# Optimization experiments

Hardware: AMD Instinct MI355X
Metric: run time of the kernel (lower is better)

## Reference

```python
import jax, jax.numpy as jnp
import numpy as np

# dims
N, BARS, F = 1024, 64, 32          # frames, bars per frame, bar features
H, HEADS, ENC_L, FFN = 256, 8, 4, 1024
HD = H // HEADS
D, DS, DC, ML = 512, 16, 4, 8      # mamba d_model, d_state, d_conv, n_layers
DI = 2 * D                          # expand=2 -> d_inner
DR = D // 16                        # dt_rank
HID = 128                           # VIX head hidden


def _ln(x, g, b, eps=1e-5):
    m = x.mean(-1, keepdims=True)
    v = ((x - m) ** 2).mean(-1, keepdims=True)
    return (x - m) * jax.lax.rsqrt(v + eps) * g + b


def setup_inputs() -> dict:
    key = jax.random.key(0)
    ks = iter(jax.random.split(key, 64))
    r = lambda *s: jax.random.normal(next(ks), s, jnp.float32) * 0.02
    inp = {}
    inp['frames'] = jax.random.normal(next(ks), (N, BARS, F), jnp.float32)
    inp['frame_mask'] = jnp.ones((N, BARS), jnp.float32)
    # bar encoder (transformer)
    inp['in_w'] = r(F, H); inp['in_b'] = jnp.zeros((H,), jnp.float32)
    inp['pos_emb'] = r(BARS, H)
    inp['enc_qkv_w'] = r(ENC_L, H, 3 * H); inp['enc_qkv_b'] = jnp.zeros((ENC_L, 3 * H), jnp.float32)
    inp['enc_attn_out_w'] = r(ENC_L, H, H); inp['enc_attn_out_b'] = jnp.zeros((ENC_L, H), jnp.float32)
    inp['enc_ln1_g'] = jnp.ones((ENC_L, H), jnp.float32); inp['enc_ln1_b'] = jnp.zeros((ENC_L, H), jnp.float32)
    inp['enc_ffn_w1'] = r(ENC_L, H, FFN); inp['enc_ffn_b1'] = jnp.zeros((ENC_L, FFN), jnp.float32)
    inp['enc_ffn_w2'] = r(ENC_L, FFN, H); inp['enc_ffn_b2'] = jnp.zeros((ENC_L, H), jnp.float32)
    inp['enc_ln2_g'] = jnp.ones((ENC_L, H), jnp.float32); inp['enc_ln2_b'] = jnp.zeros((ENC_L, H), jnp.float32)
    # projection hidden_dim -> d_model
    inp['proj_w'] = r(H, D); inp['proj_b'] = jnp.zeros((D,), jnp.float32)
    # mamba stack (stacked over ML layers)
    inp['m_in_w'] = r(ML, D, 2 * DI)
    inp['m_conv_w'] = r(ML, DI, DC); inp['m_conv_b'] = jnp.zeros((ML, DI), jnp.float32)
    inp['m_xproj_w'] = r(ML, DI, DR + 2 * DS)
    inp['m_dt_w'] = r(ML, DR, DI)
    inp['m_dt_b'] = jnp.full((ML, DI), -4.6, jnp.float32)  # softplus(-4.6)~0.01
    inp['m_Alog'] = jnp.broadcast_to(jnp.log(jnp.arange(1, DS + 1, dtype=jnp.float32)), (ML, DI, DS)) + 0.0
    inp['m_D'] = jnp.ones((ML, DI), jnp.float32)
    inp['m_out_w'] = r(ML, DI, D)
    inp['m_ln_g'] = jnp.ones((ML, D), jnp.float32); inp['m_ln_b'] = jnp.zeros((ML, D), jnp.float32)
    # attention pooling
    inp['pool_w'] = r(D, 1); inp['pool_b'] = jnp.zeros((1,), jnp.float32)
    # VIX head
    inp['h1_w'] = r(D, HID); inp['h1_b'] = jnp.zeros((HID,), jnp.float32)
    inp['hln1_g'] = jnp.ones((HID,), jnp.float32); inp['hln1_b'] = jnp.zeros((HID,), jnp.float32)
    inp['h2_w'] = r(HID, HID); inp['h2_b'] = jnp.zeros((HID,), jnp.float32)
    inp['hln2_g'] = jnp.ones((HID,), jnp.float32); inp['hln2_b'] = jnp.zeros((HID,), jnp.float32)
    inp['h3_w'] = r(HID, 1); inp['h3_b'] = jnp.zeros((1,), jnp.float32)
    return inp


def _forward(frames, frame_mask, in_w, in_b, pos_emb, enc_qkv_w, enc_qkv_b,
             enc_attn_out_w, enc_attn_out_b, enc_ln1_g, enc_ln1_b,
             enc_ffn_w1, enc_ffn_b1, enc_ffn_w2, enc_ffn_b2, enc_ln2_g, enc_ln2_b,
             proj_w, proj_b, m_in_w, m_conv_w, m_conv_b, m_xproj_w, m_dt_w, m_dt_b,
             m_Alog, m_D, m_out_w, m_ln_g, m_ln_b, pool_w, pool_b,
             h1_w, h1_b, hln1_g, hln1_b, h2_w, h2_b, hln2_g, hln2_b, h3_w, h3_b):
    # ---- bar encoder: per-frame transformer over bars ----
    x = frames @ in_w + in_b + pos_emb                        # [N,BARS,H]
    bias = (1.0 - frame_mask)[:, None, None, :] * -1e9        # key padding mask
    scale = 1.0 / np.sqrt(HD)
    for l in range(ENC_L):
        qkv = x @ enc_qkv_w[l] + enc_qkv_b[l]
        q, k, v = jnp.split(qkv, 3, axis=-1)
        q = q.reshape(N, BARS, HEADS, HD)
        k = k.reshape(N, BARS, HEADS, HD)
        v = v.reshape(N, BARS, HEADS, HD)
        att = jnp.einsum('nqhd,nkhd->nhqk', q, k) * scale + bias
        att = jax.nn.softmax(att, axis=-1)
        o = jnp.einsum('nhqk,nkhd->nqhd', att, v).reshape(N, BARS, H)
        x = _ln(x + o @ enc_attn_out_w[l] + enc_attn_out_b[l], enc_ln1_g[l], enc_ln1_b[l])
        f = jax.nn.gelu(x @ enc_ffn_w1[l] + enc_ffn_b1[l], approximate=False) @ enc_ffn_w2[l] + enc_ffn_b2[l]
        x = _ln(x + f, enc_ln2_g[l], enc_ln2_b[l])
    m = frame_mask[..., None]
    frame_emb = (x * m).sum(1) / jnp.clip(m.sum(1), 1.0)      # [N,H] masked mean pool

    # ---- project to d_model; sequence of frames is the Mamba sequence (B=1) ----
    x = frame_emb @ proj_w + proj_b                           # [T,D], T=N
    for l in range(ML):
        res = x
        xi, z = jnp.split(x @ m_in_w[l], 2, axis=-1)          # [T,DI] each
        # causal depthwise conv1d, kernel DC
        xp = jnp.pad(xi, ((DC - 1, 0), (0, 0)))
        xw = jnp.stack([xp[k:k + N] for k in range(DC)], axis=-1)  # [T,DI,DC]
        xc = jax.nn.silu((xw * m_conv_w[l]).sum(-1) + m_conv_b[l])
        xdbl = xc @ m_xproj_w[l]                               # [T,DR+2*DS]
        dtr, Bm, Cm = xdbl[:, :DR], xdbl[:, DR:DR + DS], xdbl[:, DR + DS:]
        dt = jax.nn.softplus(dtr @ m_dt_w[l] + m_dt_b[l])      # [T,DI]
        A = -jnp.exp(m_Alog[l])                                # [DI,DS]
        dA = jnp.exp(dt[:, :, None] * A)                       # [T,DI,DS]
        dBx = dt[:, :, None] * Bm[:, None, :] * xc[:, :, None] # [T,DI,DS]

        def step(h, inp):
            dA_t, dBx_t, C_t = inp
            h = h * dA_t + dBx_t
            return h, h @ C_t                                  # y_t [DI]
        _, ys = jax.lax.scan(step, jnp.zeros((DI, DS), x.dtype), (dA, dBx, Cm))
        y = (ys + m_D[l] * xc) * jax.nn.silu(z)
        x = _ln(y @ m_out_w[l], m_ln_g[l], m_ln_b[l]) + res    # layer -> norm -> +residual

    # ---- attention pooling (no mask at this stage, matches forward()) ----
    w = jax.nn.softmax(x @ pool_w + pool_b, axis=0)            # [T,1]
    hp = (w * x).sum(0)                                        # [D]
    # ---- VIX head ----
    t = jax.nn.gelu(_ln(hp @ h1_w + h1_b, hln1_g, hln1_b), approximate=False)
    t = jax.nn.gelu(_ln(t @ h2_w + h2_b, hln2_g, hln2_b), approximate=False)
    vix = t @ h3_w + h3_b                                      # [1] (batch of 1)
    return vix, x[None]                                        # vix_pred, mamba_hidden [1,T,D]


def reference(frames, frame_mask, in_w, in_b, pos_emb, enc_qkv_w, enc_qkv_b,
              enc_attn_out_w, enc_attn_out_b, enc_ln1_g, enc_ln1_b,
              enc_ffn_w1, enc_ffn_b1, enc_ffn_w2, enc_ffn_b2, enc_ln2_g, enc_ln2_b,
              proj_w, proj_b, m_in_w, m_conv_w, m_conv_b, m_xproj_w, m_dt_w, m_dt_b,
              m_Alog, m_D, m_out_w, m_ln_g, m_ln_b, pool_w, pool_b,
              h1_w, h1_b, hln1_g, hln1_b, h2_w, h2_b, hln2_g, hln2_b, h3_w, h3_b):
    return _forward(frames, frame_mask, in_w, in_b, pos_emb, enc_qkv_w, enc_qkv_b,
                    enc_attn_out_w, enc_attn_out_b, enc_ln1_g, enc_ln1_b,
                    enc_ffn_w1, enc_ffn_b1, enc_ffn_w2, enc_ffn_b2, enc_ln2_g, enc_ln2_b,
                    proj_w, proj_b, m_in_w, m_conv_w, m_conv_b, m_xproj_w, m_dt_w, m_dt_b,
                    m_Alog, m_D, m_out_w, m_ln_g, m_ln_b, pool_w, pool_b,
                    h1_w, h1_b, hln1_g, hln1_b, h2_w, h2_b, hln2_g, hln2_b, h3_w, h3_b)
```

## Files before the change

### kernel.cpp

```cpp
#include <hip/hip_runtime.h>
#include <math.h>

#define ACT_NONE 0
#define ACT_GELU 1
#define ACT_SOFTPLUS 2

template<int ACT>
__device__ __forceinline__ float act_apply(float x){
  if (ACT == ACT_GELU)     return 0.5f * x * (1.0f + erff(x * 0.70710678118654752f));
  if (ACT == ACT_SOFTPLUS) return fmaxf(x, 0.0f) + log1pf(expf(-fabsf(x)));
  return x;
}

__device__ __forceinline__ unsigned short f2bf(float x){
  unsigned u = __float_as_uint(x);
  u = u + 0x7FFFu + ((u >> 16) & 1u);
  return (unsigned short)(u >> 16);
}
__device__ __forceinline__ float bf2f(unsigned short b){
  return __uint_as_float(((unsigned)b) << 16);
}
__device__ __forceinline__ void bfsplit(float x, unsigned short &hi, unsigned short &lo){
  hi = f2bf(x);
  lo = f2bf(x - bf2f(hi));
}

typedef __attribute__((ext_vector_type(8))) short v8s;
typedef __attribute__((ext_vector_type(4))) float v4f;

template<int ACT, int OUT>
__global__ __launch_bounds__(256) void gemm_bf16x2_kernel(
    const unsigned short* __restrict__ Ahi, const unsigned short* __restrict__ Alo,
    const unsigned short* __restrict__ Bhi, const unsigned short* __restrict__ Blo,
    const float* __restrict__ bias, float* __restrict__ C,
    unsigned short* __restrict__ Chi, unsigned short* __restrict__ Clo,
    int K, int lda, int ldb, int ldc)
{
  __shared__ unsigned short As[2][128][40];
  __shared__ unsigned short Bs[2][128][40];
  const int tid = threadIdx.x;
  const int m0 = blockIdx.y * 128;
  const int n0 = blockIdx.x * 128;
  const int w = tid >> 6, lane = tid & 63;
  const int wm = (w & 1) * 64, wn = (w >> 1) * 64;
  const int fm = lane & 15, fq = lane >> 4;
  const int r = tid >> 1, h = tid & 1;

  const unsigned short* pAh = Ahi + (size_t)(m0 + r) * lda + h * 16;
  const unsigned short* pAl = Alo + (size_t)(m0 + r) * lda + h * 16;
  const unsigned short* pBh = Bhi + (size_t)(n0 + r) * ldb + h * 16;
  const unsigned short* pBl = Blo + (size_t)(n0 + r) * ldb + h * 16;

  v4f acc[4][4];
#pragma unroll
  for (int i = 0; i < 4; i++)
#pragma unroll
    for (int j = 0; j < 4; j++) acc[i][j] = (v4f){0.f, 0.f, 0.f, 0.f};

  uint4 ah0 = *(const uint4*)(pAh),     ah1 = *(const uint4*)(pAh + 8);
  uint4 al0 = *(const uint4*)(pAl),     al1 = *(const uint4*)(pAl + 8);
  uint4 bh0 = *(const uint4*)(pBh),     bh1 = *(const uint4*)(pBh + 8);
  uint4 bl0 = *(const uint4*)(pBl),     bl1 = *(const uint4*)(pBl + 8);

  for (int k0 = 0; k0 < K; k0 += 32) {
    __syncthreads();
    *(uint4*)&As[0][r][h * 16]     = ah0;
    *(uint4*)&As[0][r][h * 16 + 8] = ah1;
    *(uint4*)&As[1][r][h * 16]     = al0;
    *(uint4*)&As[1][r][h * 16 + 8] = al1;
    *(uint4*)&Bs[0][r][h * 16]     = bh0;
    *(uint4*)&Bs[0][r][h * 16 + 8] = bh1;
    *(uint4*)&Bs[1][r][h * 16]     = bl0;
    *(uint4*)&Bs[1][r][h * 16 + 8] = bl1;
    __syncthreads();

    if (k0 + 32 < K) {
      int kn = k0 + 32;
      ah0 = *(const uint4*)(pAh + kn); ah1 = *(const uint4*)(pAh + kn + 8);
      al0 = *(const uint4*)(pAl + kn); al1 = *(const uint4*)(pAl + kn + 8);
      bh0 = *(const uint4*)(pBh + kn); bh1 = *(const uint4*)(pBh + kn + 8);
      bl0 = *(const uint4*)(pBl + kn); bl1 = *(const uint4*)(pBl + kn + 8);
    }

    v8s ah[4], al[4];
#pragma unroll
    for (int i = 0; i < 4; i++) {
      ah[i] = *(const v8s*)&As[0][wm + i * 16 + fm][fq * 8];
      al[i] = *(const v8s*)&As[1][wm + i * 16 + fm][fq * 8];
    }
#pragma unroll
    for (int j = 0; j < 4; j++) {
      v8s bh = *(const v8s*)&Bs[0][wn + j * 16 + fm][fq * 8];
      v8s bl = *(const v8s*)&Bs[1][wn + j * 16 + fm][fq * 8];
#pragma unroll
      for (int i = 0; i < 4; i++) {
        acc[i][j] = __builtin_amdgcn_mfma_f32_16x16x32_bf16(ah[i], bh, acc[i][j], 0, 0, 0);
        acc[i][j] = __builtin_amdgcn_mfma_f32_16x16x32_bf16(ah[i], bl, acc[i][j], 0, 0, 0);
        acc[i][j] = __builtin_amdgcn_mfma_f32_16x16x32_bf16(al[i], bh, acc[i][j], 0, 0, 0);
      }
    }
  }

#pragma unroll
  for (int i = 0; i < 4; i++)
#pragma unroll
    for (int j = 0; j < 4; j++) {
      int col = n0 + wn + j * 16 + fm;
      float bv = bias ? bias[col] : 0.0f;
#pragma unroll
      for (int reg = 0; reg < 4; reg++) {
        int row = m0 + wm + i * 16 + fq * 4 + reg;
        float v = acc[i][j][reg] + bv;
        v = act_apply<ACT>(v);
        size_t idx = (size_t)row * ldc + col;
        if (OUT == 0) C[idx] = v;
        else { unsigned short hi, lo; bfsplit(v, hi, lo); Chi[idx] = hi; Clo[idx] = lo; }
      }
    }
}

__global__ __launch_bounds__(256) void gemm_ln_kernel(
    const unsigned short* __restrict__ Ahi, const unsigned short* __restrict__ Alo,
    const unsigned short* __restrict__ Bhi, const unsigned short* __restrict__ Blo,
    const float* __restrict__ bias,
    const float* __restrict__ g, const float* __restrict__ beta,
    unsigned short* __restrict__ Xhi, unsigned short* __restrict__ Xlo,
    int K, int lda, int ldb)
{
  __shared__ unsigned short As[2][32][40];
  __shared__ unsigned short Bs[2][256][40];
  __shared__ float rs[32][5];
  __shared__ float ms[32][2];
  const int tid = threadIdx.x;
  const int m0 = blockIdx.x * 32;
  const int w = tid >> 6, lane = tid & 63;
  const int fm = lane & 15, fq = lane >> 4;
  const int a_sel = tid >> 7;
  const int a_row = (tid >> 2) & 31;
  const int a_c   = tid & 3;
  const int b_row = tid >> 2;
  const int b_c   = tid & 3;

  v4f acc[2][4];
#pragma unroll
  for (int i = 0; i < 2; i++)
#pragma unroll
    for (int j = 0; j < 4; j++) acc[i][j] = (v4f){0.f, 0.f, 0.f, 0.f};

  for (int k0 = 0; k0 < K; k0 += 32) {
    __syncthreads();
    {
      const unsigned short* asrc = (a_sel ? Alo : Ahi) + (size_t)(m0 + a_row) * lda + k0 + a_c * 8;
      *(uint4*)&As[a_sel][a_row][a_c * 8] = *(const uint4*)asrc;
    }
#pragma unroll
    for (int p = 0; p < 4; p++) {
      int row = p * 64 + b_row;
      *(uint4*)&Bs[0][row][b_c * 8] = *(const uint4*)(Bhi + (size_t)row * ldb + k0 + b_c * 8);
      *(uint4*)&Bs[1][row][b_c * 8] = *(const uint4*)(Blo + (size_t)row * ldb + k0 + b_c * 8);
    }
    __syncthreads();

    v8s ah[2], al[2];
#pragma unroll
    for (int i = 0; i < 2; i++) {
      ah[i] = *(const v8s*)&As[0][i * 16 + fm][fq * 8];
      al[i] = *(const v8s*)&As[1][i * 16 + fm][fq * 8];
    }
#pragma unroll
    for (int j = 0; j < 4; j++) {
      v8s bhf = *(const v8s*)&Bs[0][w * 64 + j * 16 + fm][fq * 8];
      v8s blf = *(const v8s*)&Bs[1][w * 64 + j * 16 + fm][fq * 8];
#pragma unroll
      for (int i = 0; i < 2; i++) {
        acc[i][j] = __builtin_amdgcn_mfma_f32_16x16x32_bf16(ah[i], bhf, acc[i][j], 0, 0, 0);
        acc[i][j] = __builtin_amdgcn_mfma_f32_16x16x32_bf16(ah[i], blf, acc[i][j], 0, 0, 0);
        acc[i][j] = __builtin_amdgcn_mfma_f32_16x16x32_bf16(al[i], bhf, acc[i][j], 0, 0, 0);
      }
    }
  }

#pragma unroll
  for (int i = 0; i < 2; i++)
#pragma unroll
    for (int j = 0; j < 4; j++) {
      int cl = w * 64 + j * 16 + fm;
      float bv = bias[cl];
#pragma unroll
      for (int reg = 0; reg < 4; reg++) {
        int rl = i * 16 + fq * 4 + reg;
        size_t idx = (size_t)(m0 + rl) * 256 + cl;
        acc[i][j][reg] += bv + bf2f(Xhi[idx]) + bf2f(Xlo[idx]);
      }
    }
#pragma unroll
  for (int i = 0; i < 2; i++)
#pragma unroll
    for (int reg = 0; reg < 4; reg++) {
      float s = acc[i][0][reg] + acc[i][1][reg] + acc[i][2][reg] + acc[i][3][reg];
      s += __shfl_xor(s, 1); s += __shfl_xor(s, 2);
      s += __shfl_xor(s, 4); s += __shfl_xor(s, 8);
      if (fm == 0) rs[i * 16 + fq * 4 + reg][w] = s;
    }
  __syncthreads();
  if (tid < 32) ms[tid][0] = (rs[tid][0] + rs[tid][1] + rs[tid][2] + rs[tid][3]) * (1.0f / 256.0f);
  __syncthreads();
#pragma unroll
  for (int i = 0; i < 2; i++)
#pragma unroll
    for (int reg = 0; reg < 4; reg++) {
      int rl = i * 16 + fq * 4 + reg;
      float mean = ms[rl][0];
      float s = 0.0f;
#pragma unroll
      for (int j = 0; j < 4; j++) { float d = acc[i][j][reg] - mean; s += d * d; }
      s += __shfl_xor(s, 1); s += __shfl_xor(s, 2);
      s += __shfl_xor(s, 4); s += __shfl_xor(s, 8);
      if (fm == 0) rs[rl][w] = s;
    }
  __syncthreads();
  if (tid < 32) {
    float var = (rs[tid][0] + rs[tid][1] + rs[tid][2] + rs[tid][3]) * (1.0f / 256.0f);
    ms[tid][1] = rsqrtf(var + 1e-5f);
  }
  __syncthreads();
#pragma unroll
  for (int i = 0; i < 2; i++)
#pragma unroll
    for (int j = 0; j < 4; j++) {
      int cl = w * 64 + j * 16 + fm;
      float gv = g[cl], bv = beta[cl];
#pragma unroll
      for (int reg = 0; reg < 4; reg++) {
        int rl = i * 16 + fq * 4 + reg;
        float t = (acc[i][j][reg] - ms[rl][0]) * ms[rl][1] * gv + bv;
        size_t idx = (size_t)(m0 + rl) * 256 + cl;
        unsigned short hi, lo; bfsplit(t, hi, lo);
        Xhi[idx] = hi; Xlo[idx] = lo;
      }
    }
}

__global__ __launch_bounds__(256) void wsplit_kernel(
    const float* __restrict__ W, unsigned short* __restrict__ Whi,
    unsigned short* __restrict__ Wlo, int K, int N, size_t wstride, size_t ostride)
{
  __shared__ float tile[32][33];
  const float* Wl = W + blockIdx.z * wstride;
  unsigned short* Whl = Whi + blockIdx.z * ostride;
  unsigned short* Wll = Wlo + blockIdx.z * ostride;
  int k0 = blockIdx.y * 32, n0 = blockIdx.x * 32;
  int t = threadIdx.x;
  int tn = t & 31, tk8 = t >> 5;
#pragma unroll
  for (int i = 0; i < 4; i++) {
    int k = tk8 + i * 8;
    tile[k][tn] = Wl[(size_t)(k0 + k) * N + n0 + tn];
  }
  __syncthreads();
  int tk = t & 31, tn8 = t >> 5;
#pragma unroll
  for (int i = 0; i < 4; i++) {
    int n = tn8 + i * 8;
    float v = tile[tk][n];
    unsigned short hi, lo; bfsplit(v, hi, lo);
    size_t idx = (size_t)(n0 + n) * K + k0 + tk;
    Whl[idx] = hi; Wll[idx] = lo;
  }
}

template<int ACT, int POS, int SPLIT>
__global__ __launch_bounds__(256) void gemm128_kernel(
    const float* __restrict__ A, const float* __restrict__ W,
    const float* __restrict__ bias, const float* __restrict__ pos,
    float* __restrict__ C, unsigned short* __restrict__ Chi, unsigned short* __restrict__ Clo,
    int K, int lda, int ldw, int ldc)
{
  __shared__ float As[16][128];
  __shared__ float Ws[16][128];
  const int tid = threadIdx.x;
  const int m0 = blockIdx.y * 128;
  const int n0 = blockIdx.x * 128;
  const int tx = tid & 15, ty = tid >> 4;
  const int ar = tid >> 2, ak = (tid & 3) * 4;
  const int wk = tid >> 5, wn = (tid & 31) * 4;

  float acc[8][8];
#pragma unroll
  for (int i = 0; i < 8; i++)
#pragma unroll
    for (int j = 0; j < 8; j++) acc[i][j] = 0.0f;

  for (int k0 = 0; k0 < K; k0 += 16) {
    float4 a0 = *(const float4*)(A + (size_t)(m0 + ar)      * lda + k0 + ak);
    float4 a1 = *(const float4*)(A + (size_t)(m0 + ar + 64) * lda + k0 + ak);
    float4 w0 = *(const float4*)(W + (size_t)(k0 + wk)     * ldw + n0 + wn);
    float4 w1 = *(const float4*)(W + (size_t)(k0 + wk + 8) * ldw + n0 + wn);
    __syncthreads();
    As[ak + 0][ar] = a0.x; As[ak + 1][ar] = a0.y; As[ak + 2][ar] = a0.z; As[ak + 3][ar] = a0.w;
    As[ak + 0][ar + 64] = a1.x; As[ak + 1][ar + 64] = a1.y; As[ak + 2][ar + 64] = a1.z; As[ak + 3][ar + 64] = a1.w;
    *(float4*)&Ws[wk][wn] = w0;
    *(float4*)&Ws[wk + 8][wn] = w1;
    __syncthreads();
#pragma unroll
    for (int k = 0; k < 16; k++) {
      float4 xa = *(float4*)&As[k][ty * 8];
      float4 xb = *(float4*)&As[k][ty * 8 + 4];
      float4 y0 = *(float4*)&Ws[k][tx * 8];
      float4 y1 = *(float4*)&Ws[k][tx * 8 + 4];
      float a8[8] = {xa.x, xa.y, xa.z, xa.w, xb.x, xb.y, xb.z, xb.w};
      float b8[8] = {y0.x, y0.y, y0.z, y0.w, y1.x, y1.y, y1.z, y1.w};
#pragma unroll
      for (int i = 0; i < 8; i++)
#pragma unroll
        for (int j = 0; j < 8; j++) acc[i][j] = fmaf(a8[i], b8[j], acc[i][j]);
    }
  }
#pragma unroll
  for (int i = 0; i < 8; i++) {
    int row = m0 + ty * 8 + i;
    float* cp = C + (size_t)row * ldc + n0 + tx * 8;
    float v[8];
#pragma unroll
    for (int j = 0; j < 8; j++) {
      float t = acc[i][j];
      int col = n0 + tx * 8 + j;
      if (bias) t += bias[col];
      if (POS)  t += pos[(row & 63) * 256 + col];
      t = act_apply<ACT>(t);
      v[j] = t;
      if (SPLIT) {
        unsigned short hi, lo; bfsplit(t, hi, lo);
        size_t idx = (size_t)row * ldc + col;
        Chi[idx] = hi; Clo[idx] = lo;
      }
    }
    *(float4*)cp       = make_float4(v[0], v[1], v[2], v[3]);
    *(float4*)(cp + 4) = make_float4(v[4], v[5], v[6], v[7]);
  }
}

template<int ACT>
__global__ __launch_bounds__(256) void gemm64_kernel(
    const float* __restrict__ A, const float* __restrict__ W,
    const float* __restrict__ bias, float* __restrict__ C,
    int K, int lda, int ldw, int ldc)
{
  __shared__ float As[16][64];
  __shared__ float Ws[16][64];
  const int tid = threadIdx.x;
  const int m0 = blockIdx.y * 64;
  const int n0 = blockIdx.x * 64;
  const int tx = tid & 15, ty = tid >> 4;
  const int ar = tid >> 2, ak = (tid & 3) * 4;
  const int wk = tid >> 4, wn = (tid & 15) * 4;

  float acc[4][4];
#pragma unroll
  for (int i = 0; i < 4; i++)
#pragma unroll
    for (int j = 0; j < 4; j++) acc[i][j] = 0.0f;

  float4 a0 = *(const float4*)(A + (size_t)(m0 + ar) * lda + ak);
  float4 w0 = *(const float4*)(W + (size_t)wk * ldw + n0 + wn);

  for (int k0 = 0; k0 < K; k0 += 16) {
    __syncthreads();
    As[ak + 0][ar] = a0.x; As[ak + 1][ar] = a0.y; As[ak + 2][ar] = a0.z; As[ak + 3][ar] = a0.w;
    *(float4*)&Ws[wk][wn] = w0;
    __syncthreads();
    if (k0 + 16 < K) {
      a0 = *(const float4*)(A + (size_t)(m0 + ar) * lda + k0 + 16 + ak);
      w0 = *(const float4*)(W + (size_t)(k0 + 16 + wk) * ldw + n0 + wn);
    }
#pragma unroll
    for (int k = 0; k < 16; k++) {
      float4 xa = *(float4*)&As[k][ty * 4];
      float4 yb = *(float4*)&Ws[k][tx * 4];
      float a4[4] = {xa.x, xa.y, xa.z, xa.w};
      float b4[4] = {yb.x, yb.y, yb.z, yb.w};
#pragma unroll
      for (int i = 0; i < 4; i++)
#pragma unroll
        for (int j = 0; j < 4; j++) acc[i][j] = fmaf(a4[i], b4[j], acc[i][j]);
    }
  }
#pragma unroll
  for (int i = 0; i < 4; i++) {
    float* cp = C + (size_t)(m0 + ty * 4 + i) * ldc + n0 + tx * 4;
    float v[4];
#pragma unroll
    for (int j = 0; j < 4; j++) {
      float t = acc[i][j];
      if (bias) t += bias[n0 + tx * 4 + j];
      v[j] = act_apply<ACT>(t);
    }
    *(float4*)cp = make_float4(v[0], v[1], v[2], v[3]);
  }
}

__global__ __launch_bounds__(64) void attn_fused_kernel(
    const float* __restrict__ QKVc, const float* __restrict__ mask,
    unsigned short* __restrict__ AThi, unsigned short* __restrict__ ATlo, int n0)
{
  int bid = blockIdx.x;
  int nl = bid >> 3;
  int h = bid & 7;
  int n = n0 + nl;
  int tid = threadIdx.x;
  int tx = tid & 7, ty = tid >> 3;
  __shared__ float Qt[32][68];
  __shared__ float Kt[32][68];
  __shared__ float Vs[64][36];
  __shared__ float Pt[64][68];
  __shared__ float bs[64];
  const float* base = QKVc + (size_t)nl * (64 * 768);
#pragma unroll
  for (int i = 0; i < 32; i++) {
    int idx = tid + i * 64;
    int bar = idx >> 5, c = idx & 31;
    Qt[c][bar] = base[bar * 768 + h * 32 + c];
    Kt[c][bar] = base[bar * 768 + 256 + h * 32 + c];
    Vs[bar][c] = base[bar * 768 + 512 + h * 32 + c];
  }
  bs[tid] = (1.0f - mask[n * 64 + tid]) * -1e9f;
  __syncthreads();
  float acc[8][8] = {};
  for (int c = 0; c < 32; c++) {
    float4 ax = *(float4*)&Qt[c][ty * 8];
    float4 ay = *(float4*)&Qt[c][ty * 8 + 4];
    float4 bx = *(float4*)&Kt[c][tx * 8];
    float4 by = *(float4*)&Kt[c][tx * 8 + 4];
    float a8[8] = {ax.x, ax.y, ax.z, ax.w, ay.x, ay.y, ay.z, ay.w};
    float b8[8] = {bx.x, bx.y, bx.z, bx.w, by.x, by.y, by.z, by.w};
#pragma unroll
    for (int i = 0; i < 8; i++)
#pragma unroll
      for (int j = 0; j < 8; j++) acc[i][j] = fmaf(a8[i], b8[j], acc[i][j]);
  }
  const float scale = 0.17677669529663687f;
#pragma unroll
  for (int i = 0; i < 8; i++) {
    float s[8];
    float mx = -3.0e38f;
#pragma unroll
    for (int j = 0; j < 8; j++) { s[j] = acc[i][j] * scale + bs[tx * 8 + j]; mx = fmaxf(mx, s[j]); }
#pragma unroll
    for (int off = 1; off < 8; off <<= 1) mx = fmaxf(mx, __shfl_xor(mx, off));
    float sum = 0.0f;
#pragma unroll
    for (int j = 0; j < 8; j++) { s[j] = expf(s[j] - mx); sum += s[j]; }
#pragma unroll
    for (int off = 1; off < 8; off <<= 1) sum += __shfl_xor(sum, off);
    float inv = 1.0f / sum;
#pragma unroll
    for (int j = 0; j < 8; j++) Pt[tx * 8 + j][ty * 8 + i] = s[j] * inv;
  }
  __syncthreads();
  float o[8][4] = {};
  for (int j = 0; j < 64; j++) {
    float4 px = *(float4*)&Pt[j][ty * 8];
    float4 py = *(float4*)&Pt[j][ty * 8 + 4];
    float4 v  = *(float4*)&Vs[j][tx * 4];
    float p8[8] = {px.x, px.y, px.z, px.w, py.x, py.y, py.z, py.w};
#pragma unroll
    for (int i = 0; i < 8; i++) {
      o[i][0] = fmaf(p8[i], v.x, o[i][0]);
      o[i][1] = fmaf(p8[i], v.y, o[i][1]);
      o[i][2] = fmaf(p8[i], v.z, o[i][2]);
      o[i][3] = fmaf(p8[i], v.w, o[i][3]);
    }
  }
#pragma unroll
  for (int i = 0; i < 8; i++) {
    size_t base_o = (size_t)(nl * 64 + ty * 8 + i) * 256 + h * 32 + tx * 4;
#pragma unroll
    for (int c = 0; c < 4; c++) {
      unsigned short hi, lo; bfsplit(o[i][c], hi, lo);
      AThi[base_o + c] = hi; ATlo[base_o + c] = lo;
    }
  }
}

__global__ __launch_bounds__(256) void ln_res_kernel(
    const float* __restrict__ a, const float* __restrict__ b,
    const float* __restrict__ g, const float* __restrict__ beta,
    float* __restrict__ o, int Wd)
{
  int wave = threadIdx.x >> 6;
  int lane = threadIdx.x & 63;
  int row = blockIdx.x * 4 + wave;
  int P = Wd >> 6;
  const float* ar = a + (size_t)row * Wd;
  const float* br = b + (size_t)row * Wd;
  float v[8];
  float s = 0.0f;
  for (int i = 0; i < P; i++) { float x = ar[lane + i * 64]; v[i] = x; s += x; }
#pragma unroll
  for (int off = 32; off; off >>= 1) s += __shfl_xor(s, off);
  float mean = s / Wd;
  float vs = 0.0f;
  for (int i = 0; i < P; i++) { float d = v[i] - mean; vs += d * d; }
#pragma unroll
  for (int off = 32; off; off >>= 1) vs += __shfl_xor(vs, off);
  float rstd = rsqrtf(vs / Wd + 1e-5f);
  for (int i = 0; i < P; i++) {
    int col = lane + i * 64;
    o[(size_t)row * Wd + col] = (v[i] - mean) * rstd * g[col] + beta[col] + br[col];
  }
}

__global__ __launch_bounds__(256) void mean_kernel(
    const unsigned short* __restrict__ Xhi, const unsigned short* __restrict__ Xlo,
    const float* __restrict__ mask, float* __restrict__ FE, int n0)
{
  int n = blockIdx.x;
  int c = threadIdx.x;
  float s = 0.0f, ms = 0.0f;
  for (int bar = 0; bar < 64; bar++) {
    float mk = mask[(n0 + n) * 64 + bar];
    size_t idx = (size_t)(n * 64 + bar) * 256 + c;
    s = fmaf(bf2f(Xhi[idx]) + bf2f(Xlo[idx]), mk, s);
    ms += mk;
  }
  FE[(n0 + n) * 256 + c] = s / fmaxf(ms, 1.0f);
}

__global__ __launch_bounds__(256) void conv_kernel(
    const float* __restrict__ XZ, const float* __restrict__ w,
    const float* __restrict__ b, float* __restrict__ XC)
{
  int idx = blockIdx.x * 256 + threadIdx.x;
  int t = idx >> 10, c = idx & 1023;
  float acc = b[c];
  const float* wc = w + c * 4;
#pragma unroll
  for (int k = 0; k < 4; k++) {
    int tt = t + k - 3;
    if (tt >= 0) acc = fmaf(XZ[(size_t)tt * 2048 + c], wc[k], acc);
  }
  XC[idx] = acc / (1.0f + expf(-acc));
}

#define NCH 32
#define CLEN 32

__global__ __launch_bounds__(256) void scan1_kernel(
    const float* __restrict__ DT, const float* __restrict__ XC,
    const float* __restrict__ XDBL, const float* __restrict__ Alog,
    float* __restrict__ HEND, float* __restrict__ PPR)
{
  int j = blockIdx.x >> 2;
  int c = (blockIdx.x & 3) * 256 + threadIdx.x;
  int t0 = j * CLEN;
  __shared__ float Bs[CLEN][16];
  for (int i = threadIdx.x; i < CLEN * 16; i += 256) {
    int r = i >> 4, s = i & 15;
    Bs[r][s] = XDBL[(t0 + r) * 64 + 32 + s];
  }
  float A[16], h[16], Pp[16];
#pragma unroll
  for (int s = 0; s < 16; s++) {
    A[s] = -expf(Alog[c * 16 + s]);
    h[s] = 0.0f; Pp[s] = 1.0f;
  }
  __syncthreads();
  for (int tt = 0; tt < CLEN; tt++) {
    int t = t0 + tt;
    float dtv = DT[(size_t)t * 1024 + c];
    float u = dtv * XC[(size_t)t * 1024 + c];
#pragma unroll
    for (int s = 0; s < 16; s++) {
      float e = expf(dtv * A[s]);
      h[s] = fmaf(h[s], e, u * Bs[tt][s]);
      Pp[s] *= e;
    }
  }
#pragma unroll
  for (int s = 0; s < 16; s++) {
    HEND[(size_t)(j * 1024 + c) * 16 + s] = h[s];
    PPR [(size_t)(j * 1024 + c) * 16 + s] = Pp[s];
  }
}

__global__ __launch_bounds__(256) void scan2_kernel(
    const float* __restrict__ HEND, const float* __restrict__ PPR, float* __restrict__ CIN)
{
  int id = blockIdx.x * 256 + threadIdx.x;
  float carry = 0.0f;
  for (int j = 0; j < NCH; j++) {
    CIN[j * 16384 + id] = carry;
    carry = fmaf(PPR[j * 16384 + id], carry, HEND[j * 16384 + id]);
  }
}

__global__ __launch_bounds__(256) void scan3_kernel(
    const float* __restrict__ DT, const float* __restrict__ XC,
    const float* __restrict__ XDBL, const float* __restrict__ Alog,
    const float* __restrict__ CIN, const float* __restrict__ mD,
    const float* __restrict__ XZ, float* __restrict__ Y)
{
  int j = blockIdx.x >> 2;
  int c = (blockIdx.x & 3) * 256 + threadIdx.x;
  int t0 = j * CLEN;
  __shared__ float Bs[CLEN][16], Cs[CLEN][16];
  for (int i = threadIdx.x; i < CLEN * 16; i += 256) {
    int r = i >> 4, s = i & 15;
    Bs[r][s] = XDBL[(t0 + r) * 64 + 32 + s];
    Cs[r][s] = XDBL[(t0 + r) * 64 + 48 + s];
  }
  float A[16], h[16];
#pragma unroll
  for (int s = 0; s < 16; s++) {
    A[s] = -expf(Alog[c * 16 + s]);
    h[s] = CIN[(size_t)(j * 1024 + c) * 16 + s];
  }
  float dval = mD[c];
  __syncthreads();
  for (int tt = 0; tt < CLEN; tt++) {
    int t = t0 + tt;
    float dtv = DT[(size_t)t * 1024 + c];
    float xcv = XC[(size_t)t * 1024 + c];
    float u = dtv * xcv;
    float y = 0.0f;
#pragma unroll
    for (int s = 0; s < 16; s++) {
      float e = expf(dtv * A[s]);
      h[s] = fmaf(h[s], e, u * Bs[tt][s]);
      y = fmaf(h[s], Cs[tt][s], y);
    }
    float z = XZ[(size_t)t * 2048 + 1024 + c];
    float sz = z / (1.0f + expf(-z));
    Y[(size_t)t * 1024 + c] = (y + dval * xcv) * sz;
  }
}

__global__ __launch_bounds__(1024) void pool1_kernel(
    const float* __restrict__ XM, const float* __restrict__ pw,
    const float* __restrict__ pb, float* __restrict__ PW)
{
  int t = threadIdx.x;
  float s = pb[0];
  for (int i = 0; i < 512; i++) s = fmaf(XM[(size_t)t * 512 + i], pw[i], s);
  __shared__ float red[1024];
  red[t] = s;
  __syncthreads();
  for (int off = 512; off > 0; off >>= 1) {
    if (t < off) red[t] = fmaxf(red[t], red[t + off]);
    __syncthreads();
  }
  float mx = red[0];
  __syncthreads();
  float e = expf(s - mx);
  red[t] = e;
  __syncthreads();
  for (int off = 512; off > 0; off >>= 1) {
    if (t < off) red[t] = red[t] + red[t + off];
    __syncthreads();
  }
  PW[t] = e / red[0];
}

__global__ __launch_bounds__(256) void pool2_kernel(
    const float* __restrict__ XM, const float* __restrict__ PW, float* __restrict__ HP)
{
  int hcol = blockIdx.x * 256 + threadIdx.x;
  float s = 0.0f;
  for (int tn = 0; tn < 1024; tn++) s = fmaf(PW[tn], XM[(size_t)tn * 512 + hcol], s);
  HP[hcol] = s;
}

__device__ __forceinline__ float blk_reduce_sum_128(float v, float* red){
  int t = threadIdx.x;
#pragma unroll
  for (int off = 32; off; off >>= 1) v += __shfl_xor(v, off);
  __syncthreads();
  if ((t & 63) == 0) red[t >> 6] = v;
  __syncthreads();
  return red[0] + red[1];
}

__global__ __launch_bounds__(128) void head_kernel(
    const float* __restrict__ HP, const float* __restrict__ h1w, const float* __restrict__ h1b,
    const float* __restrict__ g1, const float* __restrict__ be1,
    const float* __restrict__ h2w, const float* __restrict__ h2b,
    const float* __restrict__ g2, const float* __restrict__ be2,
    const float* __restrict__ h3w, const float* __restrict__ h3b,
    float* __restrict__ out)
{
  __shared__ float t1[128];
  __shared__ float red[2];
  int i = threadIdx.x;
  float s = h1b[i];
  for (int k = 0; k < 512; k++) s = fmaf(HP[k], h1w[k * 128 + i], s);
  float mean = blk_reduce_sum_128(s, red) * (1.0f / 128.0f);
  float d = s - mean;
  float var = blk_reduce_sum_128(d * d, red) * (1.0f / 128.0f);
  float x1 = d * rsqrtf(var + 1e-5f) * g1[i] + be1[i];
  x1 = 0.5f * x1 * (1.0f + erff(x1 * 0.70710678118654752f));
  t1[i] = x1;
  __syncthreads();
  s = h2b[i];
  for (int k = 0; k < 128; k++) s = fmaf(t1[k], h2w[k * 128 + i], s);
  mean = blk_reduce_sum_128(s, red) * (1.0f / 128.0f);
  d = s - mean;
  var = blk_reduce_sum_128(d * d, red) * (1.0f / 128.0f);
  float x2 = d * rsqrtf(var + 1e-5f) * g2[i] + be2[i];
  x2 = 0.5f * x2 * (1.0f + erff(x2 * 0.70710678118654752f));
  float tot = blk_reduce_sum_128(x2 * h3w[i], red);
  if (i == 0) out[0] = tot + h3b[0];
}

__global__ __launch_bounds__(256) void copyx_kernel(const float* __restrict__ XM, float* __restrict__ out){
  int i = blockIdx.x * 256 + threadIdx.x;
  out[1 + i] = XM[i];
}

extern "C" void kernel_launch(void* const* d_in, const int* in_sizes, int n_in,
                              void* d_out, int out_size, void* d_ws, size_t ws_size,
                              hipStream_t stream)
{
  const float* frames   = (const float*)d_in[0];
  const float* fmask    = (const float*)d_in[1];
  const float* in_w     = (const float*)d_in[2];
  const float* in_b     = (const float*)d_in[3];
  const float* pos_emb  = (const float*)d_in[4];
  const float* qkv_w    = (const float*)d_in[5];
  const float* qkv_b    = (const float*)d_in[6];
  const float* ao_w     = (const float*)d_in[7];
  const float* ao_b     = (const float*)d_in[8];
  const float* ln1_g    = (const float*)d_in[9];
  const float* ln1_b    = (const float*)d_in[10];
  const float* ffn_w1   = (const float*)d_in[11];
  const float* ffn_b1   = (const float*)d_in[12];
  const float* ffn_w2   = (const float*)d_in[13];
  const float* ffn_b2   = (const float*)d_in[14];
  const float* ln2_g    = (const float*)d_in[15];
  const float* ln2_b    = (const float*)d_in[16];
  const float* proj_w   = (const float*)d_in[17];
  const float* proj_b   = (const float*)d_in[18];
  const float* m_in_w   = (const float*)d_in[19];
  const float* m_conv_w = (const float*)d_in[20];
  const float* m_conv_b = (const float*)d_in[21];
  const float* m_xproj_w= (const float*)d_in[22];
  const float* m_dt_w   = (const float*)d_in[23];
  const float* m_dt_b   = (const float*)d_in[24];
  const float* m_Alog   = (const float*)d_in[25];
  const float* m_D      = (const float*)d_in[26];
  const float* m_out_w  = (const float*)d_in[27];
  const float* m_ln_g   = (const float*)d_in[28];
  const float* m_ln_b   = (const float*)d_in[29];
  const float* pool_w   = (const float*)d_in[30];
  const float* pool_b   = (const float*)d_in[31];
  const float* h1_w     = (const float*)d_in[32];
  const float* h1_b     = (const float*)d_in[33];
  const float* hg1      = (const float*)d_in[34];
  const float* hb1      = (const float*)d_in[35];
  const float* h2_w     = (const float*)d_in[36];
  const float* h2_b     = (const float*)d_in[37];
  const float* hg2      = (const float*)d_in[38];
  const float* hb2      = (const float*)d_in[39];
  const float* h3_w     = (const float*)d_in[40];
  const float* h3_b     = (const float*)d_in[41];
  float* out = (float*)d_out;

  float* ws = (float*)d_ws;
  float* B  = ws;
  float* QF = B;
  unsigned short* AThi = (unsigned short*)(B + 12582912);
  unsigned short* ATlo = AThi + 4194304;
  unsigned short* MIDhi = (unsigned short*)B;
  unsigned short* MIDlo = MIDhi + 16777216;

  unsigned short* Xhi = (unsigned short*)(ws + 16777216);
  unsigned short* Xlo = Xhi + 4194304;

  unsigned short* Wqkv_hi = (unsigned short*)(ws + 20971520);
  unsigned short* Wqkv_lo = Wqkv_hi + 786432;
  unsigned short* Wao_hi  = Wqkv_lo + 786432;
  unsigned short* Wao_lo  = Wao_hi + 262144;
  unsigned short* Wf1_hi  = Wao_lo + 262144;
  unsigned short* Wf1_lo  = Wf1_hi + 1048576;
  unsigned short* Wf2_hi  = Wf1_lo + 1048576;
  unsigned short* Wf2_lo  = Wf2_hi + 1048576;

  float* FE = ws + 24117248;
  float* XM = FE + 262144;
  float* PW = XM + 524288;
  float* HP = PW + 2048;

  float* XZ   = B;
  float* XC   = B + 2097152;
  float* DT   = B + 3145728;
  float* XDBL = B + 4194304;
  float* Y    = B + 4259840;
  float* TMP  = B + 5308416;
  float* HEND = B + 5832704;
  float* PPR  = B + 6356992;
  float* CIN  = B + 6881280;

  wsplit_kernel<<<dim3(24,8,4),256,0,stream>>>(qkv_w, Wqkv_hi, Wqkv_lo, 256, 768, 196608, 196608);
  wsplit_kernel<<<dim3(8,8,4),256,0,stream>>>(ao_w, Wao_hi, Wao_lo, 256, 256, 65536, 65536);
  wsplit_kernel<<<dim3(32,8,4),256,0,stream>>>(ffn_w1, Wf1_hi, Wf1_lo, 256, 1024, 262144, 262144);
  wsplit_kernel<<<dim3(8,32,4),256,0,stream>>>(ffn_w2, Wf2_hi, Wf2_lo, 1024, 256, 262144, 262144);

  for (int ch = 0; ch < 4; ch++) {
    int n0 = ch * 256;
    const float* fch = frames + (size_t)n0 * 64 * 32;
    gemm128_kernel<ACT_NONE,1,1><<<dim3(2,128),256,0,stream>>>(
        fch, in_w, in_b, pos_emb, QF, Xhi, Xlo, 32, 32, 256, 256);
    for (int l = 0; l < 4; l++) {
      gemm_bf16x2_kernel<ACT_NONE,0><<<dim3(6,128),256,0,stream>>>(
          Xhi, Xlo, Wqkv_hi + l*196608, Wqkv_lo + l*196608, qkv_b + l*768,
          QF, nullptr, nullptr, 256, 256, 256, 768);
      attn_fused_kernel<<<2048,64,0,stream>>>(QF, fmask, AThi, ATlo, n0);
      gemm_ln_kernel<<<512,256,0,stream>>>(
          AThi, ATlo, Wao_hi + l*65536, Wao_lo + l*65536, ao_b + l*256,
          ln1_g + l*256, ln1_b + l*256, Xhi, Xlo, 256, 256, 256);
      gemm_bf16x2_kernel<ACT_GELU,2><<<dim3(8,128),256,0,stream>>>(
          Xhi, Xlo, Wf1_hi + l*262144, Wf1_lo + l*262144, ffn_b1 + l*1024,
          nullptr, MIDhi, MIDlo, 256, 256, 256, 1024);
      gemm_ln_kernel<<<512,256,0,stream>>>(
          MIDhi, MIDlo, Wf2_hi + l*262144, Wf2_lo + l*262144, ffn_b2 + l*256,
          ln2_g + l*256, ln2_b + l*256, Xhi, Xlo, 1024, 1024, 1024);
    }
    mean_kernel<<<256,256,0,stream>>>(Xhi, Xlo, fmask, FE, n0);
  }

  gemm64_kernel<ACT_NONE><<<dim3(8,16),256,0,stream>>>(FE, proj_w, proj_b, XM, 256, 256, 512, 512);

  for (int l = 0; l < 8; l++) {
    gemm64_kernel<ACT_NONE><<<dim3(32,16),256,0,stream>>>(
        XM, m_in_w + (size_t)l*512*2048, nullptr, XZ, 512, 512, 2048, 2048);
    conv_kernel<<<4096,256,0,stream>>>(XZ, m_conv_w + l*1024*4, m_conv_b + l*1024, XC);
    gemm64_kernel<ACT_NONE><<<dim3(1,16),256,0,stream>>>(
        XC, m_xproj_w + (size_t)l*1024*64, nullptr, XDBL, 1024, 1024, 64, 64);
    gemm64_kernel<ACT_SOFTPLUS><<<dim3(16,16),256,0,stream>>>(
        XDBL, m_dt_w + (size_t)l*32*1024, m_dt_b + l*1024, DT, 32, 64, 1024, 1024);
    scan1_kernel<<<128,256,0,stream>>>(DT, XC, XDBL, m_Alog + l*16384, HEND, PPR);
    scan2_kernel<<<64,256,0,stream>>>(HEND, PPR, CIN);
    scan3_kernel<<<128,256,0,stream>>>(DT, XC, XDBL, m_Alog + l*16384, CIN, m_D + l*1024, XZ, Y);
    gemm64_kernel<ACT_NONE><<<dim3(8,16),256,0,stream>>>(
        Y, m_out_w + (size_t)l*1024*512, nullptr, TMP, 1024, 1024, 512, 512);
    ln_res_kernel<<<256,256,0,stream>>>(TMP, XM, m_ln_g + l*512, m_ln_b + l*512, XM, 512);
  }

  pool1_kernel<<<1,1024,0,stream>>>(XM, pool_w, pool_b, PW);
  pool2_kernel<<<2,256,0,stream>>>(XM, PW, HP);
  head_kernel<<<1,128,0,stream>>>(HP, h1_w, h1_b, hg1, hb1, h2_w, h2_b, hg2, hb2, h3_w, h3_b, out);
  copyx_kernel<<<2048,256,0,stream>>>(XM, out);
}
```

Measured before the change: 5.405 ms.

## Enlarge gemm_ln tile to 64 rows with 512 threads; alias attention smem

The GEMM+LayerNorm kernel now processes 64 rows per block with 8 waves instead of 32 rows with 4 waves. Each wave covers 32 output columns over 4 row fragments, so every loaded B (weight) tile is reused across twice as many rows, halving weight traffic per output row. The row-reduction scratch grows to match. Separately, the attention kernel now reuses the Q/K shared-memory region for the probability matrix, with an added barrier, to cut LDS footprint and raise occupancy. The trade-off is half as many blocks for the LN GEMMs (256) and more registers per thread.

Result: no change. 5.392 ms (-0.3%).

```diff
diff --git a/kernel.cpp b/kernel.cpp
--- a/kernel.cpp
+++ b/kernel.cpp
@@ -119,7 +119,7 @@
     }
 }
 
-__global__ __launch_bounds__(256) void gemm_ln_kernel(
+__global__ __launch_bounds__(512) void gemm_ln_kernel(
     const unsigned short* __restrict__ Ahi, const unsigned short* __restrict__ Alo,
     const unsigned short* __restrict__ Bhi, const unsigned short* __restrict__ Blo,
     const float* __restrict__ bias,
@@ -127,52 +127,50 @@
     unsigned short* __restrict__ Xhi, unsigned short* __restrict__ Xlo,
     int K, int lda, int ldb)
 {
-  __shared__ unsigned short As[2][32][40];
+  __shared__ unsigned short As[2][64][40];
   __shared__ unsigned short Bs[2][256][40];
-  __shared__ float rs[32][5];
-  __shared__ float ms[32][2];
+  __shared__ float rs[64][9];
+  __shared__ float ms[64][2];
   const int tid = threadIdx.x;
-  const int m0 = blockIdx.x * 32;
+  const int m0 = blockIdx.x * 64;
   const int w = tid >> 6, lane = tid & 63;
   const int fm = lane & 15, fq = lane >> 4;
-  const int a_sel = tid >> 7;
-  const int a_row = (tid >> 2) & 31;
+  const int a_pl  = tid >> 8;
+  const int a_row = (tid >> 2) & 63;
   const int a_c   = tid & 3;
   const int b_row = tid >> 2;
   const int b_c   = tid & 3;
 
-  v4f acc[2][4];
-#pragma unroll
-  for (int i = 0; i < 2; i++)
-#pragma unroll
-    for (int j = 0; j < 4; j++) acc[i][j] = (v4f){0.f, 0.f, 0.f, 0.f};
+  v4f acc[4][2];
+#pragma unroll
+  for (int i = 0; i < 4; i++)
+#pragma unroll
+    for (int j = 0; j < 2; j++) acc[i][j] = (v4f){0.f, 0.f, 0.f, 0.f};
 
   for (int k0 = 0; k0 < K; k0 += 32) {
     __syncthreads();
     {
-      const unsigned short* asrc = (a_sel ? Alo : Ahi) + (size_t)(m0 + a_row) * lda + k0 + a_c * 8;
-      *(uint4*)&As[a_sel][a_row][a_c * 8] = *(const uint4*)asrc;
-    }
-#pragma unroll
-    for (int p = 0; p < 4; p++) {
-      int row = p * 64 + b_row;
-      *(uint4*)&Bs[0][row][b_c * 8] = *(const uint4*)(Bhi + (size_t)row * ldb + k0 + b_c * 8);
-      *(uint4*)&Bs[1][row][b_c * 8] = *(const uint4*)(Blo + (size_t)row * ldb + k0 + b_c * 8);
-    }
-    __syncthreads();
-
-    v8s ah[2], al[2];
-#pragma unroll
-    for (int i = 0; i < 2; i++) {
+      const unsigned short* asrc = (a_pl ? Alo : Ahi) + (size_t)(m0 + a_row) * lda + k0 + a_c * 8;
+      *(uint4*)&As[a_pl][a_row][a_c * 8] = *(const uint4*)asrc;
+    }
+    *(uint4*)&Bs[0][b_row      ][b_c * 8] = *(const uint4*)(Bhi + (size_t)(b_row      ) * ldb + k0 + b_c * 8);
+    *(uint4*)&Bs[0][b_row + 128][b_c * 8] = *(const uint4*)(Bhi + (size_t)(b_row + 128) * ldb + k0 + b_c * 8);
+    *(uint4*)&Bs[1][b_row      ][b_c * 8] = *(const uint4*)(Blo + (size_t)(b_row      ) * ldb + k0 + b_c * 8);
+    *(uint4*)&Bs[1][b_row + 128][b_c * 8] = *(const uint4*)(Blo + (size_t)(b_row + 128) * ldb + k0 + b_c * 8);
+    __syncthreads();
+
+    v8s ah[4], al[4];
+#pragma unroll
+    for (int i = 0; i < 4; i++) {
       ah[i] = *(const v8s*)&As[0][i * 16 + fm][fq * 8];
       al[i] = *(const v8s*)&As[1][i * 16 + fm][fq * 8];
     }
 #pragma unroll
-    for (int j = 0; j < 4; j++) {
-      v8s bhf = *(const v8s*)&Bs[0][w * 64 + j * 16 + fm][fq * 8];
-      v8s blf = *(const v8s*)&Bs[1][w * 64 + j * 16 + fm][fq * 8];
-#pragma unroll
-      for (int i = 0; i < 2; i++) {
+    for (int j = 0; j < 2; j++) {
+      v8s bhf = *(const v8s*)&Bs[0][w * 32 + j * 16 + fm][fq * 8];
+      v8s blf = *(const v8s*)&Bs[1][w * 32 + j * 16 + fm][fq * 8];
+#pragma unroll
+      for (int i = 0; i < 4; i++) {
         acc[i][j] = __builtin_amdgcn_mfma_f32_16x16x32_bf16(ah[i], bhf, acc[i][j], 0, 0, 0);
         acc[i][j] = __builtin_amdgcn_mfma_f32_16x16x32_bf16(ah[i], blf, acc[i][j], 0, 0, 0);
         acc[i][j] = __builtin_amdgcn_mfma_f32_16x16x32_bf16(al[i], bhf, acc[i][j], 0, 0, 0);
@@ -181,10 +179,10 @@
   }
 
 #pragma unroll
-  for (int i = 0; i < 2; i++)
-#pragma unroll
-    for (int j = 0; j < 4; j++) {
-      int cl = w * 64 + j * 16 + fm;
+  for (int i = 0; i < 4; i++)
+#pragma unroll
+    for (int j = 0; j < 2; j++) {
+      int cl = w * 32 + j * 16 + fm;
       float bv = bias[cl];
 #pragma unroll
       for (int reg = 0; reg < 4; reg++) {
@@ -194,41 +192,48 @@
       }
     }
 #pragma unroll
-  for (int i = 0; i < 2; i++)
+  for (int i = 0; i < 4; i++)
 #pragma unroll
     for (int reg = 0; reg < 4; reg++) {
-      float s = acc[i][0][reg] + acc[i][1][reg] + acc[i][2][reg] + acc[i][3][reg];
+      float s = acc[i][0][reg] + acc[i][1][reg];
       s += __shfl_xor(s, 1); s += __shfl_xor(s, 2);
       s += __shfl_xor(s, 4); s += __shfl_xor(s, 8);
       if (fm == 0) rs[i * 16 + fq * 4 + reg][w] = s;
     }
   __syncthreads();
-  if (tid < 32) ms[tid][0] = (rs[tid][0] + rs[tid][1] + rs[tid][2] + rs[tid][3]) * (1.0f / 256.0f);
-  __syncthreads();
-#pragma unroll
-  for (int i = 0; i < 2; i++)
+  if (tid < 64) {
+    float s = 0.0f;
+#pragma unroll
+    for (int q = 0; q < 8; q++) s += rs[tid][q];
+    ms[tid][0] = s * (1.0f / 256.0f);
+  }
+  __syncthreads();
+#pragma unroll
+  for (int i = 0; i < 4; i++)
 #pragma unroll
     for (int reg = 0; reg < 4; reg++) {
       int rl = i * 16 + fq * 4 + reg;
       float mean = ms[rl][0];
-      float s = 0.0f;
-#pragma unroll
-      for (int j = 0; j < 4; j++) { float d = acc[i][j][reg] - mean; s += d * d; }
+      float d0 = acc[i][0][reg] - mean;
+      float d1 = acc[i][1][reg] - mean;
+      float s = d0 * d0 + d1 * d1;
       s += __shfl_xor(s, 1); s += __shfl_xor(s, 2);
       s += __shfl_xor(s, 4); s += __shfl_xor(s, 8);
       if (fm == 0) rs[rl][w] = s;
     }
   __syncthreads();
-  if (tid < 32) {
-    float var = (rs[tid][0] + rs[tid][1] + rs[tid][2] + rs[tid][3]) * (1.0f / 256.0f);
-    ms[tid][1] = rsqrtf(var + 1e-5f);
-  }
-  __syncthreads();
-#pragma unroll
-  for (int i = 0; i < 2; i++)
-#pragma unroll
-    for (int j = 0; j < 4; j++) {
-      int cl = w * 64 + j * 16 + fm;
+  if (tid < 64) {
+    float s = 0.0f;
+#pragma unroll
+    for (int q = 0; q < 8; q++) s += rs[tid][q];
+    ms[tid][1] = rsqrtf(s * (1.0f / 256.0f) + 1e-5f);
+  }
+  __syncthreads();
+#pragma unroll
+  for (int i = 0; i < 4; i++)
+#pragma unroll
+    for (int j = 0; j < 2; j++) {
+      int cl = w * 32 + j * 16 + fm;
       float gv = g[cl], bv = beta[cl];
 #pragma unroll
       for (int reg = 0; reg < 4; reg++) {
@@ -409,10 +414,11 @@
   int n = n0 + nl;
   int tid = threadIdx.x;
   int tx = tid & 7, ty = tid >> 3;
-  __shared__ float Qt[32][68];
-  __shared__ float Kt[32][68];
+  __shared__ float QKP[4352];
+  float (*Qt)[68] = (float(*)[68])QKP;
+  float (*Kt)[68] = (float(*)[68])(QKP + 32 * 68);
+  float (*Pt)[68] = (float(*)[68])QKP;
   __shared__ float Vs[64][36];
-  __shared__ float Pt[64][68];
   __shared__ float bs[64];
   const float* base = QKVc + (size_t)nl * (64 * 768);
 #pragma unroll
@@ -438,6 +444,7 @@
 #pragma unroll
       for (int j = 0; j < 8; j++) acc[i][j] = fmaf(a8[i], b8[j], acc[i][j]);
   }
+  __syncthreads();
   const float scale = 0.17677669529663687f;
 #pragma unroll
   for (int i = 0; i < 8; i++) {
@@ -814,13 +821,13 @@
           Xhi, Xlo, Wqkv_hi + l*196608, Wqkv_lo + l*196608, qkv_b + l*768,
           QF, nullptr, nullptr, 256, 256, 256, 768);
       attn_fused_kernel<<<2048,64,0,stream>>>(QF, fmask, AThi, ATlo, n0);
-      gemm_ln_kernel<<<512,256,0,stream>>>(
+      gemm_ln_kernel<<<256,512,0,stream>>>(
           AThi, ATlo, Wao_hi + l*65536, Wao_lo + l*65536, ao_b + l*256,
           ln1_g + l*256, ln1_b + l*256, Xhi, Xlo, 256, 256, 256);
       gemm_bf16x2_kernel<ACT_GELU,2><<<dim3(8,128),256,0,stream>>>(
           Xhi, Xlo, Wf1_hi + l*262144, Wf1_lo + l*262144, ffn_b1 + l*1024,
           nullptr, MIDhi, MIDlo, 256, 256, 256, 1024);
-      gemm_ln_kernel<<<512,256,0,stream>>>(
+      gemm_ln_kernel<<<256,512,0,stream>>>(
           MIDhi, MIDlo, Wf2_hi + l*262144, Wf2_lo + l*262144, ffn_b2 + l*256,
           ln2_g + l*256, ln2_b + l*256, Xhi, Xlo, 1024, 1024, 1024);
     }
```
